# Kernel tuning notes

Measured on AMD Instinct MI355X. Metric: run time of the kernel, lower is better.

The kernel has to match this reference:

```python
import jax, jax.numpy as jnp
import numpy as np

D_IN = 1024
D_OUT = 1024


def setup_inputs() -> dict:
    key = jax.random.key(0)
    kx, kq, kk, kv = jax.random.split(key, 4)
    B, T = 8, 2048
    x = jax.random.normal(kx, (B, T, D_IN), dtype=jnp.float32)
    # torch Linear weight is (d_out, d_in); we store transposed (d_in, d_out)
    s = 1.0 / np.sqrt(D_IN)
    Wq = jax.random.uniform(kq, (D_IN, D_OUT), jnp.float32, -s, s)
    Wk = jax.random.uniform(kk, (D_IN, D_OUT), jnp.float32, -s, s)
    Wv = jax.random.uniform(kv, (D_IN, D_OUT), jnp.float32, -s, s)
    return {"x": x, "Wq": Wq, "Wk": Wk, "Wv": Wv}


def reference(x, Wq, Wk, Wv):
    # x: (B, T, d_in)
    T = x.shape[1]
    d_out = Wq.shape[1]
    q = jnp.einsum('btd,de->bte', x, Wq)  # (B,T,d_out)
    k = jnp.einsum('btd,de->bte', x, Wk)
    v = jnp.einsum('btd,de->bte', x, Wv)
    scores = jnp.einsum('bqe,bke->bqk', q, k)  # (B,T,T)
    causal = jnp.tril(jnp.ones((T, T), dtype=bool))  # True = keep
    scores = jnp.where(causal[None], scores, -jnp.inf)
    weights = jax.nn.softmax(scores / jnp.sqrt(jnp.asarray(d_out, x.dtype)), axis=-1)
    # dropout p=0.0 -> identity
    return jnp.einsum('bqk,bke->bqe', weights, v)  # (B,T,d_out)
```

## Files before the change

kernel.cpp:

```cpp
#include <hip/hip_runtime.h>

using u16 = unsigned short;
typedef __bf16 bf16x8 __attribute__((ext_vector_type(8)));
typedef unsigned short u16x8 __attribute__((ext_vector_type(8)));
typedef float floatx4 __attribute__((ext_vector_type(4)));

__device__ __forceinline__ u16 f2bf(float f) {
  union { float f; unsigned u; } c; c.f = f;
  unsigned u = c.u;
  u += 0x7fffu + ((u >> 16) & 1u);
  return (u16)(u >> 16);
}
__device__ __forceinline__ float bf2f(u16 h) {
  union { unsigned u; float f; } c; c.u = ((unsigned)h) << 16; return c.f;
}

__device__ __forceinline__ void st_out(float* p, float v) { *p = v; }
__device__ __forceinline__ void st_out(u16* p, float v) { *p = f2bf(v); }

__device__ __forceinline__ void load16(const u16* g, u16* l) {
  __builtin_amdgcn_global_load_lds(
      (const __attribute__((address_space(1))) void*)g,
      (__attribute__((address_space(3))) void*)l, 16, 0, 0);
}

#define TILE 128
#define BK 64

template<typename OutT>
__device__ __forceinline__ void gemm_core(
    const u16* __restrict__ A, int lda, long sA,
    const u16* __restrict__ Bt, int ldb, long sB,
    OutT* __restrict__ C, int ldc, long sC,
    int kmax, int bx, int by, int bz, int tid)
{
  __shared__ u16 As[TILE * BK];
  __shared__ u16 Bs[TILE * BK];

  const u16* Ab = A + bz * sA + (long)by * TILE * lda;
  const u16* Bb = Bt + bz * sB + (long)bx * TILE * ldb;

  int lane = tid & 63;
  int wm = ((tid >> 7) & 1) * 64;
  int wn = ((tid >> 6) & 1) * 64;

  floatx4 acc[4][4] = {};
  int arow = wm + (lane & 15);
  int brow = wn + (lane & 15);
  int q = lane >> 4;

  for (int k0 = 0; k0 < kmax; k0 += BK) {
    __syncthreads();
#pragma unroll
    for (int h = 0; h < 4; h++) {
      int cc = tid + h * 256;
      int row = cc >> 3, gm = (cc & 7) ^ (row & 7);
      load16(Ab + (long)row * lda + k0 + gm * 8, &As[cc * 8]);
    }
#pragma unroll
    for (int h = 0; h < 4; h++) {
      int cc = tid + h * 256;
      int row = cc >> 3, gm = (cc & 7) ^ (row & 7);
      load16(Bb + (long)row * ldb + k0 + gm * 8, &Bs[cc * 8]);
    }
    __builtin_amdgcn_s_waitcnt(0);
    __syncthreads();

#pragma unroll
    for (int kp = 0; kp < 2; kp++) {
      bf16x8 a[4], b[4];
#pragma unroll
      for (int i = 0; i < 4; i++) {
        int r = arow + i * 16;
        a[i] = *(const bf16x8*)&As[(r * 8 + ((kp * 4 + q) ^ (r & 7))) * 8];
      }
#pragma unroll
      for (int j = 0; j < 4; j++) {
        int r = brow + j * 16;
        b[j] = *(const bf16x8*)&Bs[(r * 8 + ((kp * 4 + q) ^ (r & 7))) * 8];
      }
#pragma unroll
      for (int i = 0; i < 4; i++)
#pragma unroll
        for (int j = 0; j < 4; j++)
          acc[i][j] = __builtin_amdgcn_mfma_f32_16x16x32_bf16(a[i], b[j], acc[i][j], 0, 0, 0);
    }
  }

  OutT* Cb = C + bz * sC;
  int colbase = bx * TILE + wn + (lane & 15);
  int rowbase = by * TILE + wm + ((lane >> 4) << 2);
#pragma unroll
  for (int i = 0; i < 4; i++)
#pragma unroll
    for (int j = 0; j < 4; j++) {
      int col = colbase + j * 16;
#pragma unroll
      for (int r = 0; r < 4; r++)
        st_out(&Cb[(long)(rowbase + i * 16 + r) * ldc + col], acc[i][j][r]);
    }
}

template<typename OutT>
__global__ __launch_bounds__(256, 2)
void gemm_rect(const u16* __restrict__ A, int lda, long sA,
               const u16* __restrict__ Bt, int ldb, long sB,
               OutT* __restrict__ C, int ldc, long sC, int K,
               int l2gx, int nO8s)
{
  int L = blockIdx.x;
  int t = ((L & 7) << nO8s) | (L >> 3);
  int bx = t & ((1 << l2gx) - 1), by = t >> l2gx;
  gemm_core<OutT>(A, lda, sA, Bt, ldb, sB, C, ldc, sC, K, bx, by, blockIdx.y, threadIdx.x);
}

__global__ __launch_bounds__(256, 2)
void gemm_proj(const u16* __restrict__ xb, const u16* __restrict__ NT,
               const u16* __restrict__ WvT, u16* __restrict__ Yb,
               u16* __restrict__ VT)
{
  int L = blockIdx.x;
  bool h = (L >= 1024);
  int LL = h ? L - 1024 : L;
  int t = ((LL & 7) << 7) | (LL >> 3);
  int bx = h ? (t & 127) : (t & 7);
  int by = h ? (t >> 7) : (t >> 3);
  gemm_core<u16>(h ? WvT : xb, 1024, 0L,
                 h ? xb : NT, 1024, 0L,
                 h ? VT : Yb, h ? 16384 : 1024, 0L,
                 1024, bx, by, 0, threadIdx.x);
}

__global__ __launch_bounds__(256, 2)
void gemm_tri(const u16* __restrict__ A, int lda, long sA,
              const u16* __restrict__ Bt, int ldb, long sB,
              u16* __restrict__ C, int ldc, long sC, int K)
{
  int tp = blockIdx.x;
  int t = (tp & 7) * 17 + (tp >> 3);
  int r = (int)((sqrtf(8.f * t + 1.f) - 1.f) * 0.5f);
  while ((r + 1) * (r + 2) / 2 <= t) ++r;
  while (r * (r + 1) / 2 > t) --r;
  int c = t - r * (r + 1) / 2;
  gemm_core<u16>(A, lda, sA, Bt, ldb, sB, C, ldc, sC, K, c, r, blockIdx.y, threadIdx.x);
}

__global__ __launch_bounds__(256, 2)
void gemm_opv(const u16* __restrict__ P, int lda, long sA,
              const u16* __restrict__ VT, int ldb, long sB,
              float* __restrict__ C, int ldc, long sC)
{
  int L = blockIdx.x;
  int j = L & 7, s = L >> 3;
  int by = (s < 8) ? 15 - j : j;
  int bx = s & 7;
  gemm_core<float>(P, lda, sA, VT, ldb, sB, C, ldc, sC,
                   (by + 1) * TILE, bx, by, blockIdx.y, threadIdx.x);
}

__global__ __launch_bounds__(256)
void cvt_x(const float4* __restrict__ x, u16* __restrict__ o, int n4, float scale)
{
  int i = blockIdx.x * 256 + threadIdx.x;
  if (i >= n4) return;
  float4 v = x[i];
  ushort4 r;
  r.x = f2bf(v.x * scale); r.y = f2bf(v.y * scale);
  r.z = f2bf(v.z * scale); r.w = f2bf(v.w * scale);
  *(ushort4*)(o + (long)i * 4) = r;
}

__global__ __launch_bounds__(256)
void cvt_w(const float* __restrict__ W, u16* __restrict__ O)
{
  const int D = 1024;
  __shared__ float t[64][65];
  int tid = threadIdx.x;
  int c = tid & 63, r = tid >> 6;
  int e0 = blockIdx.x * 64, d0 = blockIdx.y * 64;
  for (int rr = r; rr < 64; rr += 4)
    t[rr][c] = W[(long)(d0 + rr) * D + e0 + c];
  __syncthreads();
  for (int rr = r; rr < 64; rr += 4)
    O[(long)(e0 + rr) * D + d0 + c] = f2bf(t[c][rr]);
}

__global__ __launch_bounds__(256)
void softmax_bf16(u16* __restrict__ S)
{
  const int T = 2048;
  int row = blockIdx.x & (T - 1);
  u16* Prow = S + (long)blockIdx.x * T;
  int n = row + 1;
  int tid = threadIdx.x, lane = tid & 63, wid = tid >> 6;
  int i0 = tid * 8;

  u16x8 pv = *(const u16x8*)(Prow + i0);
  float v[8];
  float lmax = -3.0e38f;
#pragma unroll
  for (int j = 0; j < 8; j++) {
    v[j] = (i0 + j < n) ? bf2f(pv[j]) : -3.0e38f;
    lmax = fmaxf(lmax, v[j]);
  }
  __shared__ float red[8];
#pragma unroll
  for (int o = 32; o > 0; o >>= 1) lmax = fmaxf(lmax, __shfl_down(lmax, o, 64));
  if (lane == 0) red[wid] = lmax;
  __syncthreads();
  float m = fmaxf(fmaxf(red[0], red[1]), fmaxf(red[2], red[3]));

  float lsum = 0.f;
#pragma unroll
  for (int j = 0; j < 8; j++) {
    float e = (i0 + j < n) ? __expf(v[j] - m) : 0.f;
    v[j] = e;
    lsum += e;
  }
#pragma unroll
  for (int o = 32; o > 0; o >>= 1) lsum += __shfl_down(lsum, o, 64);
  if (lane == 0) red[4 + wid] = lsum;
  __syncthreads();
  float inv = 1.0f / (red[4] + red[5] + red[6] + red[7]);

  u16x8 w;
#pragma unroll
  for (int j = 0; j < 8; j++) w[j] = f2bf(v[j] * inv);
  *(u16x8*)(Prow + i0) = w;
}

extern "C" void kernel_launch(void* const* d_in, const int* in_sizes, int n_in,
                              void* d_out, int out_size, void* d_ws, size_t ws_size,
                              hipStream_t stream)
{
  const int B = 8, T = 2048, D = 1024;
  const float* x  = (const float*)d_in[0];
  const float* Wq = (const float*)d_in[1];
  const float* Wk = (const float*)d_in[2];
  const float* Wv = (const float*)d_in[3];
  float* out = (float*)d_out;
  char* ws = (char*)d_ws;

  u16* xb  = (u16*)(ws);
  u16* WvT = (u16*)(ws + (32ul << 20));
  u16* NT  = (u16*)(ws + (34ul << 20));
  u16* Yb  = (u16*)(ws + (36ul << 20));
  u16* Wqb = Yb;
  u16* Wkb = (u16*)(ws + (38ul << 20));
  u16* VT  = (u16*)(ws + (68ul << 20));
  u16* S   = (u16*)(ws + (100ul << 20));

  const size_t OFF_S = 100ul << 20;
  int NB = 8;
  while (NB > 1 && OFF_S + (size_t)NB * T * T * 2 > ws_size) NB >>= 1;

  cvt_x<<<(B * T * D / 4 + 255) / 256, 256, 0, stream>>>((const float4*)x, xb, B * T * D / 4, 1.0f);
  cvt_x<<<(D * D / 4 + 255) / 256, 256, 0, stream>>>((const float4*)Wq, Wqb, D * D / 4, 0.03125f);
  cvt_x<<<(D * D / 4 + 255) / 256, 256, 0, stream>>>((const float4*)Wk, Wkb, D * D / 4, 1.0f);
  cvt_w<<<dim3(16, 16), 256, 0, stream>>>(Wv, WvT);

  gemm_rect<u16><<<dim3(64, 1), 256, 0, stream>>>(
      Wkb, D, 0L, Wqb, D, 0L, NT, D, 0L, D, 3, 3);
  gemm_proj<<<dim3(2048, 1), 256, 0, stream>>>(xb, NT, WvT, Yb, VT);

  for (int b0 = 0; b0 < B; b0 += NB) {
    gemm_tri<<<dim3(136, NB), 256, 0, stream>>>(
        Yb + (long)b0 * T * D, D, (long)T * D,
        xb + (long)b0 * T * D, D, (long)T * D,
        S, T, (long)T * T, D);
    softmax_bf16<<<NB * T, 256, 0, stream>>>(S);
    gemm_opv<<<dim3(128, NB), 256, 0, stream>>>(
        S, T, (long)T * T,
        VT + (long)b0 * T, B * T, (long)T,
        out + (long)b0 * T * D, D, (long)T * D);
  }
}
```

Before: 372.6 us.

## Replace projection GEMM with 256x256-tile double-buffered 8-wave kernel

The fused Q/K-folded and V projection GEMM moves from 128x128 tiles with 256 threads to 256x256 tiles with 512 threads. It uses 128KB of dynamic LDS split into two buffers, so the next k-slice can load while the current one is being multiplied. Loads are interleaved between MFMA phases, with barriers and s_setprio raising priority during math. The larger tiles give more data reuse per LDS load and hide global latency. The cost is more LDS per block, which limits occupancy to about one block per CU, and 512 tiles per launch, which may leave CUs unevenly loaded.

```diff
diff --git a/kernel.cpp b/kernel.cpp
--- a/kernel.cpp
+++ b/kernel.cpp
@@ -112,23 +112,6 @@
   int t = ((L & 7) << nO8s) | (L >> 3);
   int bx = t & ((1 << l2gx) - 1), by = t >> l2gx;
   gemm_core<OutT>(A, lda, sA, Bt, ldb, sB, C, ldc, sC, K, bx, by, blockIdx.y, threadIdx.x);
-}
-
-__global__ __launch_bounds__(256, 2)
-void gemm_proj(const u16* __restrict__ xb, const u16* __restrict__ NT,
-               const u16* __restrict__ WvT, u16* __restrict__ Yb,
-               u16* __restrict__ VT)
-{
-  int L = blockIdx.x;
-  bool h = (L >= 1024);
-  int LL = h ? L - 1024 : L;
-  int t = ((LL & 7) << 7) | (LL >> 3);
-  int bx = h ? (t & 127) : (t & 7);
-  int by = h ? (t >> 7) : (t >> 3);
-  gemm_core<u16>(h ? WvT : xb, 1024, 0L,
-                 h ? xb : NT, 1024, 0L,
-                 h ? VT : Yb, h ? 16384 : 1024, 0L,
-                 1024, bx, by, 0, threadIdx.x);
 }
 
 __global__ __launch_bounds__(256, 2)
@@ -156,6 +139,176 @@
   int bx = s & 7;
   gemm_core<float>(P, lda, sA, VT, ldb, sB, C, ldc, sC,
                    (by + 1) * TILE, bx, by, blockIdx.y, threadIdx.x);
+}
+
+template<typename OutT>
+__device__ __forceinline__ void gemm_core256(
+    const u16* __restrict__ A, int lda, long sA,
+    const u16* __restrict__ Bt, int ldb, long sB,
+    OutT* __restrict__ C, int ldc, long sC,
+    int kmax, int bx, int by, int bz, int tid, u16* lds)
+{
+  const u16* Ab = A + bz * sA + (long)by * 256 * lda;
+  const u16* Bb = Bt + bz * sB + (long)bx * 256 * ldb;
+
+  const int lane = tid & 63, wid = tid >> 6;
+  const int wm = wid >> 2;
+  const int wn = wid & 3;
+  const int l15 = lane & 15, q = lane >> 4;
+
+  const int cc0 = tid, cc1 = tid + 512;
+  const int r0 = cc0 >> 3, g0 = (cc0 & 7) ^ (r0 & 7);
+  const int r1 = cc1 >> 3, g1 = (cc1 & 7) ^ (r1 & 7);
+
+  const int NK = kmax >> 6;
+
+  floatx4 acc[8][4] = {};
+
+  auto STAGE_A = [&](int k, int half, int buf) {
+    const u16* g = Ab + (long)(half * 128) * lda + k * 64;
+    load16(g + (long)r0 * lda + g0 * 8, lds + buf + half * 8192 + cc0 * 8);
+    load16(g + (long)r1 * lda + g1 * 8, lds + buf + half * 8192 + cc1 * 8);
+  };
+  auto STAGE_B = [&](int k, int half, int buf) {
+    const u16* g = Bb + (long)(half * 128) * ldb + k * 64;
+    load16(g + (long)r0 * ldb + g0 * 8, lds + buf + 16384 + half * 8192 + cc0 * 8);
+    load16(g + (long)r1 * ldb + g1 * 8, lds + buf + 16384 + half * 8192 + cc1 * 8);
+  };
+
+  STAGE_B(0, 0, 0); STAGE_B(0, 1, 0);
+  STAGE_A(0, 0, 0); STAGE_A(0, 1, 0);
+  if (NK > 1) {
+    STAGE_B(1, 0, 32768); STAGE_B(1, 1, 32768);
+    STAGE_A(1, 0, 32768);
+    asm volatile("s_waitcnt vmcnt(6)" ::: "memory");
+  } else {
+    asm volatile("s_waitcnt vmcnt(0)" ::: "memory");
+  }
+  __builtin_amdgcn_s_barrier();
+
+  const int s0 = (q ^ (l15 & 7)) * 8;
+  const int s1 = ((q + 4) ^ (l15 & 7)) * 8;
+
+  for (int k = 0; k < NK; ++k) {
+    const int buf = (k & 1) ? 32768 : 0;
+    const int nbuf = 32768 - buf;
+    const int abase = buf + wm * 8192 + l15 * 64;
+    const int bbase = buf + 16384 + (wn >> 1) * 8192 + ((wn & 1) * 64 + l15) * 64;
+
+    bf16x8 a[2][4], b[2][4];
+
+#pragma unroll
+    for (int i = 0; i < 4; ++i) {
+      a[0][i] = *(const bf16x8*)&lds[abase + i * 1024 + s0];
+      a[1][i] = *(const bf16x8*)&lds[abase + i * 1024 + s1];
+    }
+#pragma unroll
+    for (int j = 0; j < 4; ++j) {
+      b[0][j] = *(const bf16x8*)&lds[bbase + j * 1024 + s0];
+      b[1][j] = *(const bf16x8*)&lds[bbase + j * 1024 + s1];
+    }
+    if (k + 1 < NK) STAGE_A(k + 1, 1, nbuf);
+    asm volatile("" ::: "memory");
+    __builtin_amdgcn_s_barrier();
+    asm volatile("s_waitcnt lgkmcnt(0)" ::: "memory");
+    __builtin_amdgcn_s_setprio(1);
+#pragma unroll
+    for (int kp = 0; kp < 2; ++kp)
+#pragma unroll
+      for (int i = 0; i < 4; ++i)
+#pragma unroll
+        for (int j = 0; j < 2; ++j)
+          acc[i][j] = __builtin_amdgcn_mfma_f32_16x16x32_bf16(a[kp][i], b[kp][j], acc[i][j], 0, 0, 0);
+    __builtin_amdgcn_s_setprio(0);
+    asm volatile("" ::: "memory");
+    __builtin_amdgcn_s_barrier();
+
+    if (k + 2 < NK) STAGE_B(k + 2, 0, buf);
+    asm volatile("" ::: "memory");
+    __builtin_amdgcn_s_barrier();
+    __builtin_amdgcn_s_setprio(1);
+#pragma unroll
+    for (int kp = 0; kp < 2; ++kp)
+#pragma unroll
+      for (int i = 0; i < 4; ++i)
+#pragma unroll
+        for (int j = 2; j < 4; ++j)
+          acc[i][j] = __builtin_amdgcn_mfma_f32_16x16x32_bf16(a[kp][i], b[kp][j], acc[i][j], 0, 0, 0);
+    __builtin_amdgcn_s_setprio(0);
+    asm volatile("" ::: "memory");
+    __builtin_amdgcn_s_barrier();
+
+#pragma unroll
+    for (int i = 0; i < 4; ++i) {
+      a[0][i] = *(const bf16x8*)&lds[abase + 4096 + i * 1024 + s0];
+      a[1][i] = *(const bf16x8*)&lds[abase + 4096 + i * 1024 + s1];
+    }
+    if (k + 2 < NK) STAGE_B(k + 2, 1, buf);
+    asm volatile("" ::: "memory");
+    __builtin_amdgcn_s_barrier();
+    asm volatile("s_waitcnt lgkmcnt(0)" ::: "memory");
+    __builtin_amdgcn_s_setprio(1);
+#pragma unroll
+    for (int kp = 0; kp < 2; ++kp)
+#pragma unroll
+      for (int i = 0; i < 4; ++i)
+#pragma unroll
+        for (int j = 0; j < 2; ++j)
+          acc[4 + i][j] = __builtin_amdgcn_mfma_f32_16x16x32_bf16(a[kp][i], b[kp][j], acc[4 + i][j], 0, 0, 0);
+    __builtin_amdgcn_s_setprio(0);
+    asm volatile("" ::: "memory");
+    __builtin_amdgcn_s_barrier();
+
+    if (k + 2 < NK) {
+      STAGE_A(k + 2, 0, buf);
+      asm volatile("s_waitcnt vmcnt(6)" ::: "memory");
+    } else {
+      asm volatile("s_waitcnt vmcnt(0)" ::: "memory");
+    }
+    __builtin_amdgcn_s_barrier();
+    __builtin_amdgcn_s_setprio(1);
+#pragma unroll
+    for (int kp = 0; kp < 2; ++kp)
+#pragma unroll
+      for (int i = 0; i < 4; ++i)
+#pragma unroll
+        for (int j = 2; j < 4; ++j)
+          acc[4 + i][j] = __builtin_amdgcn_mfma_f32_16x16x32_bf16(a[kp][i], b[kp][j], acc[4 + i][j], 0, 0, 0);
+    __builtin_amdgcn_s_setprio(0);
+    asm volatile("" ::: "memory");
+    __builtin_amdgcn_s_barrier();
+  }
+
+  OutT* Cb = C + bz * sC;
+  const int colbase = bx * 256 + wn * 64 + l15;
+  const int rowbase = by * 256 + wm * 128 + (q << 2);
+#pragma unroll
+  for (int i = 0; i < 8; ++i)
+#pragma unroll
+    for (int j = 0; j < 4; ++j) {
+      const int col = colbase + j * 16;
+#pragma unroll
+      for (int r = 0; r < 4; ++r)
+        st_out(&Cb[(long)(rowbase + i * 16 + r) * ldc + col], acc[i][j][r]);
+    }
+}
+
+__global__ __launch_bounds__(512, 2)
+void gemm256_proj(const u16* __restrict__ xb, const u16* __restrict__ NT,
+                  const u16* __restrict__ WvT, u16* __restrict__ Yb,
+                  u16* __restrict__ VT)
+{
+  extern __shared__ u16 lds[];
+  int L = blockIdx.x;
+  int t = ((L & 7) << 6) | (L >> 3);
+  bool h = (t >= 256);
+  int tt = h ? (t - 256) : t;
+  int bx = h ? (tt & 63) : (tt & 3);
+  int by = h ? (tt >> 6) : (tt >> 2);
+  gemm_core256<u16>(h ? WvT : xb, 1024, 0L,
+                    h ? xb : NT, 1024, 0L,
+                    h ? VT : Yb, h ? 16384 : 1024, 0L,
+                    1024, bx, by, 0, (int)threadIdx.x, lds);
 }
 
 __global__ __launch_bounds__(256)
@@ -254,6 +407,13 @@
   int NB = 8;
   while (NB > 1 && OFF_S + (size_t)NB * T * T * 2 > ws_size) NB >>= 1;
 
+  static bool attr_done = false;
+  if (!attr_done) {
+    hipFuncSetAttribute(reinterpret_cast<const void*>(gemm256_proj),
+                        hipFuncAttributeMaxDynamicSharedMemorySize, 131072);
+    attr_done = true;
+  }
+
   cvt_x<<<(B * T * D / 4 + 255) / 256, 256, 0, stream>>>((const float4*)x, xb, B * T * D / 4, 1.0f);
   cvt_x<<<(D * D / 4 + 255) / 256, 256, 0, stream>>>((const float4*)Wq, Wqb, D * D / 4, 0.03125f);
   cvt_x<<<(D * D / 4 + 255) / 256, 256, 0, stream>>>((const float4*)Wk, Wkb, D * D / 4, 1.0f);
@@ -261,7 +421,7 @@
 
   gemm_rect<u16><<<dim3(64, 1), 256, 0, stream>>>(
       Wkb, D, 0L, Wqb, D, 0L, NT, D, 0L, D, 3, 3);
-  gemm_proj<<<dim3(2048, 1), 256, 0, stream>>>(xb, NT, WvT, Yb, VT);
+  gemm256_proj<<<dim3(512, 1), 512, 131072, stream>>>(xb, NT, WvT, Yb, VT);
 
   for (int b0 = 0; b0 < B; b0 += NB) {
     gemm_tri<<<dim3(136, NB), 256, 0, stream>>>(
```

Result: no change. 372.2 us (-0.1%).
